# Performance work log

Hardware: AMD Instinct MI355X
Metric: run time of the kernel (lower is better)

## Reference

```python
import jax, jax.numpy as jnp
import numpy as np
from jax.scipy.linalg import expm

N_WIRES = 9
N_LAYERS = 4
EMBED = 512
BATCH = 64
D = 2 ** N_WIRES
P = N_WIRES * N_LAYERS * 2  # gate angles per sample


def _apply_gate(st, g, w):
    # st: (D, 2,...,2) complex64; apply 2x2 gate g on wire w
    st = jnp.moveaxis(st, 1 + w, -1)
    st = st @ g.T  # new[a] = sum_b g[a,b] old[b]
    return jnp.moveaxis(st, -1, 1 + w)


def _apply_cnot(st, c, t):
    st = jnp.moveaxis(st, (1 + c, 1 + t), (-2, -1))
    st = jnp.concatenate([st[..., 0:1, :], st[..., 1:2, ::-1]], axis=-2)
    return jnp.moveaxis(st, (-2, -1), (1 + c, 1 + t))


def _build_unitary(params):
    # simulate circuit on all D basis states at once (identity input)
    st = jnp.eye(D, dtype=jnp.complex64).reshape((D,) + (2,) * N_WIRES)
    idx = 0
    for _ in range(N_LAYERS):
        for w in range(N_WIRES):
            thy = params[idx]
            thz = params[idx + 1]
            idx += 2
            c = jnp.cos(thy * 0.5).astype(jnp.complex64)
            s = jnp.sin(thy * 0.5).astype(jnp.complex64)
            ry = jnp.stack([jnp.stack([c, -s]), jnp.stack([s, c])])
            ep = jnp.exp(0.5j * thz.astype(jnp.complex64))  # exp(i*thz/2)
            zero = jnp.zeros((), jnp.complex64)
            rz = jnp.stack([jnp.stack([jnp.conj(ep), zero]), jnp.stack([zero, ep])])
            st = _apply_gate(st, rz @ ry, w)  # Ry then Rz, fused
        for w in range(N_WIRES - 1):
            st = _apply_cnot(st, w, w + 1)
        st = _apply_cnot(st, N_WIRES - 1, 0)  # ring entangler (n_wires>1)
    # row index = input basis state i -> column i of U; take real part
    return jnp.real(st.reshape(D, D)).T


def _forward(t, w1, b1, w2, b2):
    h = jax.nn.silu(t[:, None] @ w1 + b1)          # (B, EMBED)
    params = h @ w2 + b2                            # (B, P)
    p_sg = jax.lax.stop_gradient(params)            # torch uses .detach() for the circuit
    U_stack = jax.vmap(_build_unitary)(p_sg)        # (B, D, D)
    B = t.shape[0]
    A = jnp.zeros((B, D * D), params.dtype).at[:, :P].set(params).reshape(B, D, D)
    A_skew = (A - jnp.swapaxes(A, -1, -2)) * 0.01
    U_diff = jax.vmap(expm)(A_skew)                 # (B, D, D)
    return jnp.einsum('bij,bjk->bik', U_stack, U_diff)


def setup_inputs() -> dict:
    key = jax.random.key(0)
    k_t, k1, kb1, k2, kb2 = jax.random.split(key, 5)
    t = jax.random.normal(k_t, (BATCH,), jnp.float32)
    w1 = jax.random.normal(k1, (1, EMBED), jnp.float32)
    b1 = jax.random.normal(kb1, (EMBED,), jnp.float32) * 0.1
    w2 = jax.random.normal(k2, (EMBED, P), jnp.float32) / np.sqrt(EMBED)
    b2 = jax.random.normal(kb2, (P,), jnp.float32) * 0.1
    return {"t": t, "w1": w1, "b1": b1, "w2": w2, "b2": b2}


def reference(t, w1, b1, w2, b2):
    return _forward(t, w1, b1, w2, b2)
```

## Files before the change

### kernel.cpp

```cpp
#include <hip/hip_runtime.h>
#include <math.h>


__device__ __forceinline__ float2 cmul(float2 a, float2 b){
  return make_float2(fmaf(a.x, b.x, -a.y*b.y), fmaf(a.x, b.y, a.y*b.x));
}

__device__ __forceinline__ float2 pk_fma_s_lo(float2 s2, float2 b, float2 c){
  float2 d;
  asm("v_pk_fma_f32 %0, %1, %2, %3 op_sel:[0,0,0] op_sel_hi:[0,1,1]"
      : "=v"(d) : "s"(s2), "v"(b), "v"(c));
  return d;
}
__device__ __forceinline__ float2 pk_mul_s_hi(float2 s2, float2 b){
  float2 d;
  asm("v_pk_mul_f32 %0, %1, %2 op_sel:[1,0] op_sel_hi:[1,1]"
      : "=v"(d) : "s"(s2), "v"(b));
  return d;
}
__device__ __forceinline__ float2 pk_fma_vs_lo(float2 a, float2 b, float2 c){
  float2 d;
  asm("v_pk_fma_f32 %0, %1, %2, %3 op_sel:[0,0,0] op_sel_hi:[0,1,1]"
      : "=v"(d) : "v"(a), "s"(b), "v"(c));
  return d;
}
__device__ __forceinline__ float2 pk_mul_vs_hi(float2 a, float2 b){
  float2 d;
  asm("v_pk_mul_f32 %0, %1, %2 op_sel:[1,0] op_sel_hi:[1,1]"
      : "=v"(d) : "v"(a), "s"(b));
  return d;
}
__device__ __forceinline__ float2 pk_fma_vv_lo(float2 a, float2 b, float2 c){
  float2 d;
  asm("v_pk_fma_f32 %0, %1, %2, %3 op_sel:[0,0,0] op_sel_hi:[0,1,1]"
      : "=v"(d) : "v"(a), "v"(b), "v"(c));
  return d;
}
__device__ __forceinline__ float2 pk_mul_vv_hi(float2 a, float2 b){
  float2 d;
  asm("v_pk_mul_f32 %0, %1, %2 op_sel:[1,0] op_sel_hi:[1,1]"
      : "=v"(d) : "v"(a), "v"(b));
  return d;
}
__device__ __forceinline__ float2 pk_swapneg(float2 c, float2 n){
  float2 d;
  asm("v_pk_mul_f32 %0, %1, %2 op_sel:[1,0] op_sel_hi:[0,1]"
      : "=v"(d) : "v"(c), "v"(n));
  return d;
}

__device__ __forceinline__ int Fperm(int x){
  int S = x ^ (x >> 1); S ^= S >> 2; S ^= S >> 4; S ^= S >> 8;
  return (S & 0xFF) | ((((x >> 8) ^ S) & 1) << 8);
}
__device__ __forceinline__ int physmap(int x){ return x ^ ((x >> 4) & 15); }

template<int STRIDE>
__device__ __forceinline__ void apply_rot(float2 amp[8], const float2* rp){
  const float2 R0 = rp[0];
  const float2 R1 = rp[1];
  #pragma unroll
  for (int b = 0; b < 8; ++b){
    if (b & STRIDE) continue;
    const float2 u = amp[b], v = amp[b + STRIDE];
    amp[b]          = pk_fma_s_lo(R0, u, pk_mul_s_hi(R0, v));
    amp[b + STRIDE] = pk_fma_s_lo(R1, u, pk_mul_s_hi(R1, v));
  }
}

__global__ __launch_bounds__(576)
void prep_kernel(const float* __restrict__ t,  const float* __restrict__ w1,
                 const float* __restrict__ b1, const float* __restrict__ w2,
                 const float* __restrict__ b2, float* __restrict__ prep){
  __shared__ float sh[512];
  __shared__ float part[8][72];
  __shared__ float spar[72];
  const int s = blockIdx.x;
  const float ts = t[s];
  for (int k = threadIdx.x; k < 512; k += 576){
    const float z = fmaf(ts, w1[k], b1[k]);
    sh[k] = z / (1.f + expf(-z));
  }
  __syncthreads();
  {
    const int p = threadIdx.x % 72, c = threadIdx.x / 72;
    float acc = 0.f;
    const int k0 = c*64;
    for (int k = k0; k < k0 + 64; ++k) acc = fmaf(sh[k], w2[k*72 + p], acc);
    part[c][p] = acc;
  }
  __syncthreads();
  if (threadIdx.x < 72){
    const int p = threadIdx.x;
    float acc = b2[p];
    #pragma unroll
    for (int c = 0; c < 8; ++c) acc += part[c][p];
    spar[p] = acc;
  }
  __syncthreads();
  float* pb = prep + s*1024;
  const int tid = threadIdx.x;
  if (tid < 192){
    const int l = tid >> 6, m = tid & 63;
    float2 acc = make_float2(1.f, 0.f);
    #pragma unroll
    for (int w = 3; w < 9; ++w){
      const float thz = spar[2*(9*(l+1) + w) + 1];
      float zi, zr; sincosf(0.5f*thz, &zi, &zr);
      const int bit = (m >> (8 - w)) & 1;
      acc = cmul(acc, make_float2(zr, bit ? zi : -zi));
    }
    pb[128 + l*256 + 128 + m*2]     = acc.x;
    pb[128 + l*256 + 128 + m*2 + 1] = acc.y;
  } else if (tid < 216){
    const int q = tid - 192, l = q >> 3, j = q & 7;
    float2 acc = make_float2(1.f, 0.f);
    #pragma unroll
    for (int w = 0; w < 3; ++w){
      const float thz = spar[2*(9*(l+1) + w) + 1];
      float zi, zr; sincosf(0.5f*thz, &zi, &zr);
      const int bit = (j >> (2 - w)) & 1;
      acc = cmul(acc, make_float2(zr, bit ? zi : -zi));
    }
    float* o = pb + 128 + l*256 + 64 + j*4;
    o[0] = acc.x; o[1] = acc.y; o[2] = -acc.y; o[3] = acc.x;
  } else if (tid < 243){
    const int q = tid - 216, l = q / 9, w = q - l*9;
    const float thy = spar[2*(9*(l+1) + w)];
    float sy, cy; sincosf(0.5f*thy, &sy, &cy);
    float* o = pb + 128 + l*256 + w*4;
    o[0] = cy; o[1] = -sy; o[2] = sy; o[3] = cy;
  } else if (tid < 252){
    const int w = tid - 243;
    const float thy = spar[2*w], thz = spar[2*w + 1];
    float sy, cy, zi, zr;
    sincosf(0.5f*thy, &sy, &cy);
    sincosf(0.5f*thz, &zi, &zr);
    float* o = pb + w*8;
    o[0] =  zr*cy; o[1] = -zi*cy;
    o[2] = -zr*sy; o[3] =  zi*sy;
    o[4] =  zr*sy; o[5] =  zi*sy;
    o[6] =  zr*cy; o[7] =  zi*cy;
  } else if (tid < 324){
    const int j = tid - 252;
    pb[896 + j] = (j == 0) ? 0.f : 0.01f*spar[j];
  } else if (tid == 324){
    float th2 = 0.f;
    for (int j = 1; j < 72; ++j){ const float v = 0.01f*spar[j]; th2 = fmaf(v, v, th2); }
    const float th = sqrtf(th2);
    float alpha, beta;
    if (th > 1e-6f){
      alpha = sinf(th)/th;
      const float s2 = sinf(0.5f*th);
      beta = 2.f*s2*s2/th2;
    } else { alpha = 1.f - th2/6.f; beta = 0.5f; }
    pb[968] = cosf(th);
    pb[969] = alpha;
    pb[970] = beta;
  }
}

__global__ __launch_bounds__(512, 8)
void sim_kernel(const float* __restrict__ prep, float* __restrict__ out){
  __shared__ __align__(16) float2 st[8][512];
  const int s    = blockIdx.x & 63;
  const int cb   = blockIdx.x >> 6;
  const int wid  = threadIdx.x >> 6;
  const int lane = threadIdx.x & 63;
  const int col  = cb*8 + wid;
  const float* gp = prep + s*1024;
  float2* const S = st[wid];
  const float2 NEG1P1 = make_float2(-1.f, 1.f);

  float2 amp[8];
  {
    float2 base = make_float2(1.f, 0.f);
    #pragma unroll
    for (int w = 0; w < 6; ++w){
      const int xb = (lane >> (5 - w)) & 1;
      const int ib = (col  >> (8 - w)) & 1;
      const float2 ge = *(const float2*)(gp + 8*w + (xb*2 + ib)*2);
      base = cmul(base, ge);
    }
    const int i6 = (col >> 2) & 1, i7 = (col >> 1) & 1, i8 = col & 1;
    float2 G6[2], G7[2], G8[2];
    #pragma unroll
    for (int r = 0; r < 2; ++r){
      G6[r] = *(const float2*)(gp + 8*6 + (r*2 + i6)*2);
      G7[r] = *(const float2*)(gp + 8*7 + (r*2 + i7)*2);
      G8[r] = *(const float2*)(gp + 8*8 + (r*2 + i8)*2);
    }
    #pragma unroll
    for (int j = 0; j < 8; ++j){
      const float2 tj = cmul(cmul(G6[(j>>2)&1], G7[(j>>1)&1]), G8[j&1]);
      amp[j] = cmul(base, tj);
    }
    const int bFI = physmap(Fperm(lane << 3));
    #pragma unroll
    for (int j = 0; j < 8; ++j) S[bFI ^ physmap(Fperm(j))] = amp[j];
  }

  const int base1 = (lane << 3) ^ ((lane >> 1) & 15);
  const int hq = lane >> 3, lq = lane & 7;
  const int base2 = (hq << 6) ^ ((hq << 2) & 15) ^ lq;
  const int base3 = lane ^ (lane >> 4);
  const int baseF = physmap(Fperm(lane));

  #pragma unroll
  for (int L = 0; L < 3; ++L){
    const float* lb = gp + 128 + L*256;
    #pragma unroll
    for (int j = 0; j < 8; ++j) amp[j] = S[base1 ^ j];
    apply_rot<4>(amp, (const float2*)(lb + 6*4));
    apply_rot<2>(amp, (const float2*)(lb + 7*4));
    apply_rot<1>(amp, (const float2*)(lb + 8*4));
    #pragma unroll
    for (int j = 0; j < 8; ++j) S[base1 ^ j] = amp[j];
    #pragma unroll
    for (int j = 0; j < 8; ++j) amp[j] = S[base2 ^ ((j << 3) ^ (j >> 1))];
    apply_rot<4>(amp, (const float2*)(lb + 3*4));
    apply_rot<2>(amp, (const float2*)(lb + 4*4));
    apply_rot<1>(amp, (const float2*)(lb + 5*4));
    #pragma unroll
    for (int j = 0; j < 8; ++j) S[base2 ^ ((j << 3) ^ (j >> 1))] = amp[j];
    #pragma unroll
    for (int j = 0; j < 8; ++j) amp[j] = S[base3 ^ ((j << 6) ^ ((4*j) & 15))];
    apply_rot<4>(amp, (const float2*)(lb + 0*4));
    apply_rot<2>(amp, (const float2*)(lb + 1*4));
    apply_rot<1>(amp, (const float2*)(lb + 2*4));
    {
      const float2 A = *(const float2*)(lb + 128 + lane*2);
      #pragma unroll
      for (int j = 0; j < 8; ++j){
        const float2 P = *(const float2*)(lb + 64 + j*4);
        const float2 Q = *(const float2*)(lb + 64 + j*4 + 2);
        const float2 C = pk_fma_vs_lo(A, P, pk_mul_vs_hi(A, Q));
        const float2 Dn = pk_swapneg(C, NEG1P1);
        amp[j] = pk_fma_vv_lo(amp[j], C, pk_mul_vv_hi(amp[j], Dn));
      }
    }
    #pragma unroll
    for (int j = 0; j < 8; ++j) S[baseF ^ physmap(Fperm(j << 6))] = amp[j];
  }

  __syncthreads();
  #pragma unroll
  for (int rep = 0; rep < 2; ++rep){
    const int a  = (threadIdx.x >> 1) + rep*256;
    const int q  = threadIdx.x & 1;
    const int pa = a ^ ((a >> 4) & 15);
    float4 vv;
    vv.x = st[q*4 + 0][pa].x;
    vv.y = st[q*4 + 1][pa].x;
    vv.z = st[q*4 + 2][pa].x;
    vv.w = st[q*4 + 3][pa].x;
    *(float4*)&out[(size_t)s*262144 + (size_t)a*512 + cb*8 + q*4] = vv;
  }
}

__global__ __launch_bounds__(288)
void corr_kernel(const float* __restrict__ prep, float* __restrict__ out){
  __shared__ float part[16][18];
  __shared__ float srow[16][2];
  const int s  = blockIdx.x >> 5;
  const int rg = blockIdx.x & 31;
  const float* pp = prep + s*1024;
  const int lr = threadIdx.x / 18;
  const int q  = threadIdx.x - lr*18;
  float* rowp = out + (size_t)s*262144 + (size_t)(rg*16 + lr)*512;
  const float4 x  = *(const float4*)(rowp + q*4);
  const float4 vv = *(const float4*)(pp + 896 + q*4);
  part[lr][q] = fmaf(x.x,vv.x, fmaf(x.y,vv.y, fmaf(x.z,vv.z, x.w*vv.w)));
  __syncthreads();
  if (threadIdx.x < 16){
    const int row = threadIdx.x;
    float uv = 0.f;
    #pragma unroll
    for (int k = 0; k < 18; ++k) uv += part[row][k];
    const float u0 = out[(size_t)s*262144 + (size_t)(rg*16 + row)*512];
    const float cth = pp[968], alpha = pp[969], beta = pp[970];
    srow[row][0] = fmaf(alpha, u0, -beta*uv);
    srow[row][1] = cth*u0 - alpha*uv;
  }
  __syncthreads();
  const float w = srow[lr][0];
  float4 o;
  o.x = fmaf(w, vv.x, x.x); o.y = fmaf(w, vv.y, x.y);
  o.z = fmaf(w, vv.z, x.z); o.w = fmaf(w, vv.w, x.w);
  if (q == 0) o.x = srow[lr][1];
  *(float4*)(rowp + q*4) = o;
}

extern "C" void kernel_launch(void* const* d_in, const int* in_sizes, int n_in,
                              void* d_out, int out_size, void* d_ws, size_t ws_size,
                              hipStream_t stream){
  const float* t  = (const float*)d_in[0];
  const float* w1 = (const float*)d_in[1];
  const float* b1 = (const float*)d_in[2];
  const float* w2 = (const float*)d_in[3];
  const float* b2 = (const float*)d_in[4];
  float* out  = (float*)d_out;
  float* prep = (float*)d_ws;
  prep_kernel<<<64,   576, 0, stream>>>(t, w1, b1, w2, b2, prep);
  sim_kernel <<<4096, 512, 0, stream>>>(prep, out);
  corr_kernel<<<2048, 288, 0, stream>>>(prep, out);
}
```

Before: 148.5 us.

## Fold low-rank expm correction into sim kernel via precomputed U·u and U·v vectors

The prep kernel now simulates the circuit on the two vectors e0 and v, using its own shared-memory state, to get U·e0 and U·v. From these it precomputes per-row correction weights, so the sim kernel can add the rank-2 expm correction directly when it writes the first 72 columns. This removes the separate corr_kernel pass that re-read and rewrote the whole output and needed per-row reductions. It also stores gate entries in a duplicated layout so the sim kernel can use packed FMAs. The cost is more serial work in the 64-block prep kernel and a larger workspace footprint.

```diff
diff --git a/kernel.cpp b/kernel.cpp
--- a/kernel.cpp
+++ b/kernel.cpp
@@ -1,6 +1,14 @@
 #include <hip/hip_runtime.h>
 #include <math.h>
 
+
+#define PSTRIDE 2560
+#define GD_OFF  0
+#define SC_OFF  144
+#define L_OFF(l) (160 + (l)*256)
+#define V_OFF   1184
+#define W_OFF   1280
+#define C0_OFF  1792
 
 __device__ __forceinline__ float2 cmul(float2 a, float2 b){
   return make_float2(fmaf(a.x, b.x, -a.y*b.y), fmaf(a.x, b.y, a.y*b.x));
@@ -55,17 +63,67 @@
 }
 __device__ __forceinline__ int physmap(int x){ return x ^ ((x >> 4) & 15); }
 
-template<int STRIDE>
-__device__ __forceinline__ void apply_rot(float2 amp[8], const float2* rp){
-  const float2 R0 = rp[0];
-  const float2 R1 = rp[1];
+template<int STRIDE, bool UNIF>
+__device__ __forceinline__ void apply_rot(float2 amp[8], const float* rp){
+  const float2 R0 = ((const float2*)rp)[0];
+  const float2 R1 = ((const float2*)rp)[1];
   #pragma unroll
   for (int b = 0; b < 8; ++b){
     if (b & STRIDE) continue;
     const float2 u = amp[b], v = amp[b + STRIDE];
-    amp[b]          = pk_fma_s_lo(R0, u, pk_mul_s_hi(R0, v));
-    amp[b + STRIDE] = pk_fma_s_lo(R1, u, pk_mul_s_hi(R1, v));
-  }
+    if constexpr (UNIF){
+      amp[b]          = pk_fma_s_lo(R0, u, pk_mul_s_hi(R0, v));
+      amp[b + STRIDE] = pk_fma_s_lo(R1, u, pk_mul_s_hi(R1, v));
+    } else {
+      amp[b]          = pk_fma_vv_lo(R0, u, pk_mul_vv_hi(R0, v));
+      amp[b + STRIDE] = pk_fma_vv_lo(R1, u, pk_mul_vv_hi(R1, v));
+    }
+  }
+}
+
+template<bool UNIF>
+__device__ __forceinline__ void run_layer(float2* __restrict__ S,
+    const float* __restrict__ lb, const int lane,
+    const int base1, const int base2, const int base3, const int baseF,
+    const float2 NEG1P1){
+  float2 amp[8];
+  #pragma unroll
+  for (int j = 0; j < 8; ++j) amp[j] = S[base1 ^ j];
+  apply_rot<4, UNIF>(amp, lb + 6*4);
+  apply_rot<2, UNIF>(amp, lb + 7*4);
+  apply_rot<1, UNIF>(amp, lb + 8*4);
+  #pragma unroll
+  for (int j = 0; j < 8; ++j) S[base1 ^ j] = amp[j];
+  #pragma unroll
+  for (int j = 0; j < 8; ++j) amp[j] = S[base2 ^ ((j << 3) ^ (j >> 1))];
+  apply_rot<4, UNIF>(amp, lb + 3*4);
+  apply_rot<2, UNIF>(amp, lb + 4*4);
+  apply_rot<1, UNIF>(amp, lb + 5*4);
+  #pragma unroll
+  for (int j = 0; j < 8; ++j) S[base2 ^ ((j << 3) ^ (j >> 1))] = amp[j];
+  #pragma unroll
+  for (int j = 0; j < 8; ++j) amp[j] = S[base3 ^ ((j << 6) ^ ((4*j) & 15))];
+  apply_rot<4, UNIF>(amp, lb + 0*4);
+  apply_rot<2, UNIF>(amp, lb + 1*4);
+  apply_rot<1, UNIF>(amp, lb + 2*4);
+  {
+    const float2 A  = *(const float2*)(lb + 128 + lane*2);
+    const float2 A2 = pk_swapneg(A, NEG1P1);
+    #pragma unroll
+    for (int j = 0; j < 8; ++j)
+      amp[j] = pk_fma_vv_lo(amp[j], A, pk_mul_vv_hi(amp[j], A2));
+    #pragma unroll
+    for (int j = 0; j < 8; ++j){
+      const float2 P = *(const float2*)(lb + 64 + j*4);
+      const float2 Q = *(const float2*)(lb + 64 + j*4 + 2);
+      if constexpr (UNIF)
+        amp[j] = pk_fma_vs_lo(amp[j], P, pk_mul_vs_hi(amp[j], Q));
+      else
+        amp[j] = pk_fma_vv_lo(amp[j], P, pk_mul_vv_hi(amp[j], Q));
+    }
+  }
+  #pragma unroll
+  for (int j = 0; j < 8; ++j) S[baseF ^ physmap(Fperm(j << 6))] = amp[j];
 }
 
 __global__ __launch_bounds__(576)
@@ -75,6 +133,9 @@
   __shared__ float sh[512];
   __shared__ float part[8][72];
   __shared__ float spar[72];
+  __shared__ float tl[4][256];
+  __shared__ float ssc[3];
+  __shared__ __align__(16) float2 vst[2][512];
   const int s = blockIdx.x;
   const float ts = t[s];
   for (int k = threadIdx.x; k < 512; k += 576){
@@ -98,53 +159,61 @@
     spar[p] = acc;
   }
   __syncthreads();
-  float* pb = prep + s*1024;
+  float* pb = prep + (size_t)s*PSTRIDE;
   const int tid = threadIdx.x;
-  if (tid < 192){
+  if (tid < 256){
     const int l = tid >> 6, m = tid & 63;
     float2 acc = make_float2(1.f, 0.f);
     #pragma unroll
     for (int w = 3; w < 9; ++w){
-      const float thz = spar[2*(9*(l+1) + w) + 1];
+      const float thz = spar[2*(9*l + w) + 1];
       float zi, zr; sincosf(0.5f*thz, &zi, &zr);
       const int bit = (m >> (8 - w)) & 1;
       acc = cmul(acc, make_float2(zr, bit ? zi : -zi));
     }
-    pb[128 + l*256 + 128 + m*2]     = acc.x;
-    pb[128 + l*256 + 128 + m*2 + 1] = acc.y;
-  } else if (tid < 216){
-    const int q = tid - 192, l = q >> 3, j = q & 7;
+    pb[L_OFF(l) + 128 + 2*m]     = acc.x;
+    pb[L_OFF(l) + 128 + 2*m + 1] = acc.y;
+    tl[l][128 + 2*m]     = acc.x;
+    tl[l][128 + 2*m + 1] = acc.y;
+  } else if (tid < 288){
+    const int q = tid - 256, l = q >> 3, j = q & 7;
     float2 acc = make_float2(1.f, 0.f);
     #pragma unroll
     for (int w = 0; w < 3; ++w){
-      const float thz = spar[2*(9*(l+1) + w) + 1];
+      const float thz = spar[2*(9*l + w) + 1];
       float zi, zr; sincosf(0.5f*thz, &zi, &zr);
       const int bit = (j >> (2 - w)) & 1;
       acc = cmul(acc, make_float2(zr, bit ? zi : -zi));
     }
-    float* o = pb + 128 + l*256 + 64 + j*4;
+    float* o = pb + L_OFF(l) + 64 + j*4;
     o[0] = acc.x; o[1] = acc.y; o[2] = -acc.y; o[3] = acc.x;
-  } else if (tid < 243){
-    const int q = tid - 216, l = q / 9, w = q - l*9;
-    const float thy = spar[2*(9*(l+1) + w)];
+    float* o2 = &tl[l][64 + j*4];
+    o2[0] = acc.x; o2[1] = acc.y; o2[2] = -acc.y; o2[3] = acc.x;
+  } else if (tid < 324){
+    const int q = tid - 288, l = q / 9, w = q - l*9;
+    const float thy = spar[2*(9*l + w)];
     float sy, cy; sincosf(0.5f*thy, &sy, &cy);
-    float* o = pb + 128 + l*256 + w*4;
+    float* o = pb + L_OFF(l) + w*4;
     o[0] = cy; o[1] = -sy; o[2] = sy; o[3] = cy;
-  } else if (tid < 252){
-    const int w = tid - 243;
+    float* o2 = &tl[l][w*4];
+    o2[0] = cy; o2[1] = -sy; o2[2] = sy; o2[3] = cy;
+  } else if (tid < 333){
+    const int w = tid - 324;
     const float thy = spar[2*w], thz = spar[2*w + 1];
     float sy, cy, zi, zr;
     sincosf(0.5f*thy, &sy, &cy);
     sincosf(0.5f*thz, &zi, &zr);
-    float* o = pb + w*8;
-    o[0] =  zr*cy; o[1] = -zi*cy;
-    o[2] = -zr*sy; o[3] =  zi*sy;
-    o[4] =  zr*sy; o[5] =  zi*sy;
-    o[6] =  zr*cy; o[7] =  zi*cy;
-  } else if (tid < 324){
-    const int j = tid - 252;
-    pb[896 + j] = (j == 0) ? 0.f : 0.01f*spar[j];
-  } else if (tid == 324){
+    const float gr[4] = { zr*cy, -zr*sy, zr*sy, zr*cy };
+    const float gi[4] = { -zi*cy, zi*sy, zi*sy, zi*cy };
+    float* o = pb + GD_OFF + w*16;
+    #pragma unroll
+    for (int e = 0; e < 4; ++e){
+      o[e*4+0] = gr[e]; o[e*4+1] = gi[e]; o[e*4+2] = -gi[e]; o[e*4+3] = gr[e];
+    }
+  } else if (tid < 405){
+    const int j = tid - 333;
+    pb[V_OFF + j] = (j == 0) ? 0.f : 0.01f*spar[j];
+  } else if (tid == 405){
     float th2 = 0.f;
     for (int j = 1; j < 72; ++j){ const float v = 0.01f*spar[j]; th2 = fmaf(v, v, th2); }
     const float th = sqrtf(th2);
@@ -154,9 +223,41 @@
       const float s2 = sinf(0.5f*th);
       beta = 2.f*s2*s2/th2;
     } else { alpha = 1.f - th2/6.f; beta = 0.5f; }
-    pb[968] = cosf(th);
-    pb[969] = alpha;
-    pb[970] = beta;
+    pb[SC_OFF+0] = cosf(th);
+    pb[SC_OFF+1] = alpha;
+    pb[SC_OFF+2] = beta;
+    ssc[0] = cosf(th); ssc[1] = alpha; ssc[2] = beta;
+  }
+  __syncthreads();
+  if (tid < 128){
+    const int wv = tid >> 6, lane = tid & 63;
+    float2* const S = vst[wv];
+    const float2 NEG1P1 = make_float2(-1.f, 1.f);
+    const int base1 = (lane << 3) ^ ((lane >> 1) & 15);
+    const int hq = lane >> 3, lq = lane & 7;
+    const int base2 = (hq << 6) ^ ((hq << 2) & 15) ^ lq;
+    const int base3 = lane ^ (lane >> 4);
+    const int baseF = physmap(Fperm(lane));
+    #pragma unroll
+    for (int j = 0; j < 8; ++j){
+      const int x = (lane << 3) + j;
+      float re;
+      if (wv == 0) re = (x == 0) ? 1.f : 0.f;
+      else         re = (x >= 1 && x < 72) ? 0.01f*spar[x] : 0.f;
+      S[base1 ^ j] = make_float2(re, 0.f);
+    }
+    #pragma unroll
+    for (int L = 0; L < 4; ++L)
+      run_layer<false>(S, &tl[L][0], lane, base1, base2, base3, baseF, NEG1P1);
+  }
+  __syncthreads();
+  if (tid < 512){
+    const int a  = tid;
+    const int pa = a ^ ((a >> 4) & 15);
+    const float u0 = vst[0][pa].x;
+    const float uv = vst[1][pa].x;
+    pb[W_OFF  + a] = fmaf(ssc[1], u0, -ssc[2]*uv);
+    pb[C0_OFF + a] = fmaf(ssc[0], u0, -ssc[1]*uv);
   }
 }
 
@@ -168,7 +269,7 @@
   const int wid  = threadIdx.x >> 6;
   const int lane = threadIdx.x & 63;
   const int col  = cb*8 + wid;
-  const float* gp = prep + s*1024;
+  const float* gp = prep + (size_t)s*PSTRIDE;
   float2* const S = st[wid];
   const float2 NEG1P1 = make_float2(-1.f, 1.f);
 
@@ -179,21 +280,37 @@
     for (int w = 0; w < 6; ++w){
       const int xb = (lane >> (5 - w)) & 1;
       const int ib = (col  >> (8 - w)) & 1;
-      const float2 ge = *(const float2*)(gp + 8*w + (xb*2 + ib)*2);
-      base = cmul(base, ge);
+      const float4 gd = *(const float4*)(gp + GD_OFF + w*16 + (xb*2 + ib)*4);
+      const float2 d1 = make_float2(gd.x, gd.y);
+      const float2 d2 = make_float2(gd.z, gd.w);
+      base = pk_fma_vv_lo(base, d1, pk_mul_vv_hi(base, d2));
     }
     const int i6 = (col >> 2) & 1, i7 = (col >> 1) & 1, i8 = col & 1;
-    float2 G6[2], G7[2], G8[2];
+    float2 g6[2]; float4 g7d[2], g8d[2];
     #pragma unroll
     for (int r = 0; r < 2; ++r){
-      G6[r] = *(const float2*)(gp + 8*6 + (r*2 + i6)*2);
-      G7[r] = *(const float2*)(gp + 8*7 + (r*2 + i7)*2);
-      G8[r] = *(const float2*)(gp + 8*8 + (r*2 + i8)*2);
-    }
+      g6[r]  = *(const float2*)(gp + GD_OFF + 6*16 + (r*2 + i6)*4);
+      g7d[r] = *(const float4*)(gp + GD_OFF + 7*16 + (r*2 + i7)*4);
+      g8d[r] = *(const float4*)(gp + GD_OFF + 8*16 + (r*2 + i8)*4);
+    }
+    float2 g67[4];
+    #pragma unroll
+    for (int a = 0; a < 2; ++a){
+      #pragma unroll
+      for (int b = 0; b < 2; ++b){
+        const float2 d1 = make_float2(g7d[b].x, g7d[b].y);
+        const float2 d2 = make_float2(g7d[b].z, g7d[b].w);
+        g67[a*2+b] = pk_fma_vv_lo(g6[a], d1, pk_mul_vv_hi(g6[a], d2));
+      }
+    }
+    const float2 bd2 = pk_swapneg(base, NEG1P1);
     #pragma unroll
     for (int j = 0; j < 8; ++j){
-      const float2 tj = cmul(cmul(G6[(j>>2)&1], G7[(j>>1)&1]), G8[j&1]);
-      amp[j] = cmul(base, tj);
+      const float4 g8 = g8d[j & 1];
+      const float2 e1 = make_float2(g8.x, g8.y);
+      const float2 e2 = make_float2(g8.z, g8.w);
+      const float2 T  = pk_fma_vv_lo(g67[j >> 1], e1, pk_mul_vv_hi(g67[j >> 1], e2));
+      amp[j] = pk_fma_vv_lo(T, base, pk_mul_vv_hi(T, bd2));
     }
     const int bFI = physmap(Fperm(lane << 3));
     #pragma unroll
@@ -206,44 +323,14 @@
   const int base3 = lane ^ (lane >> 4);
   const int baseF = physmap(Fperm(lane));
 
-  #pragma unroll
-  for (int L = 0; L < 3; ++L){
-    const float* lb = gp + 128 + L*256;
-    #pragma unroll
-    for (int j = 0; j < 8; ++j) amp[j] = S[base1 ^ j];
-    apply_rot<4>(amp, (const float2*)(lb + 6*4));
-    apply_rot<2>(amp, (const float2*)(lb + 7*4));
-    apply_rot<1>(amp, (const float2*)(lb + 8*4));
-    #pragma unroll
-    for (int j = 0; j < 8; ++j) S[base1 ^ j] = amp[j];
-    #pragma unroll
-    for (int j = 0; j < 8; ++j) amp[j] = S[base2 ^ ((j << 3) ^ (j >> 1))];
-    apply_rot<4>(amp, (const float2*)(lb + 3*4));
-    apply_rot<2>(amp, (const float2*)(lb + 4*4));
-    apply_rot<1>(amp, (const float2*)(lb + 5*4));
-    #pragma unroll
-    for (int j = 0; j < 8; ++j) S[base2 ^ ((j << 3) ^ (j >> 1))] = amp[j];
-    #pragma unroll
-    for (int j = 0; j < 8; ++j) amp[j] = S[base3 ^ ((j << 6) ^ ((4*j) & 15))];
-    apply_rot<4>(amp, (const float2*)(lb + 0*4));
-    apply_rot<2>(amp, (const float2*)(lb + 1*4));
-    apply_rot<1>(amp, (const float2*)(lb + 2*4));
-    {
-      const float2 A = *(const float2*)(lb + 128 + lane*2);
-      #pragma unroll
-      for (int j = 0; j < 8; ++j){
-        const float2 P = *(const float2*)(lb + 64 + j*4);
-        const float2 Q = *(const float2*)(lb + 64 + j*4 + 2);
-        const float2 C = pk_fma_vs_lo(A, P, pk_mul_vs_hi(A, Q));
-        const float2 Dn = pk_swapneg(C, NEG1P1);
-        amp[j] = pk_fma_vv_lo(amp[j], C, pk_mul_vv_hi(amp[j], Dn));
-      }
-    }
-    #pragma unroll
-    for (int j = 0; j < 8; ++j) S[baseF ^ physmap(Fperm(j << 6))] = amp[j];
-  }
-
-  __syncthreads();
+  run_layer<true>(S, gp + L_OFF(1), lane, base1, base2, base3, baseF, NEG1P1);
+  run_layer<true>(S, gp + L_OFF(2), lane, base1, base2, base3, baseF, NEG1P1);
+  run_layer<true>(S, gp + L_OFF(3), lane, base1, base2, base3, baseF, NEG1P1);
+
+  __syncthreads();
+  const float* wt  = gp + W_OFF;
+  const float* c0t = gp + C0_OFF;
+  const float* vt  = gp + V_OFF;
   #pragma unroll
   for (int rep = 0; rep < 2; ++rep){
     const int a  = (threadIdx.x >> 1) + rep*256;
@@ -254,41 +341,17 @@
     vv.y = st[q*4 + 1][pa].x;
     vv.z = st[q*4 + 2][pa].x;
     vv.w = st[q*4 + 3][pa].x;
+    if (cb < 9){
+      const float  wa = wt[a];
+      const float4 vj = *(const float4*)(vt + cb*8 + q*4);
+      vv.x = fmaf(wa, vj.x, vv.x);
+      vv.y = fmaf(wa, vj.y, vv.y);
+      vv.z = fmaf(wa, vj.z, vv.z);
+      vv.w = fmaf(wa, vj.w, vv.w);
+      if ((cb | q) == 0) vv.x = c0t[a];
+    }
     *(float4*)&out[(size_t)s*262144 + (size_t)a*512 + cb*8 + q*4] = vv;
   }
-}
-
-__global__ __launch_bounds__(288)
-void corr_kernel(const float* __restrict__ prep, float* __restrict__ out){
-  __shared__ float part[16][18];
-  __shared__ float srow[16][2];
-  const int s  = blockIdx.x >> 5;
-  const int rg = blockIdx.x & 31;
-  const float* pp = prep + s*1024;
-  const int lr = threadIdx.x / 18;
-  const int q  = threadIdx.x - lr*18;
-  float* rowp = out + (size_t)s*262144 + (size_t)(rg*16 + lr)*512;
-  const float4 x  = *(const float4*)(rowp + q*4);
-  const float4 vv = *(const float4*)(pp + 896 + q*4);
-  part[lr][q] = fmaf(x.x,vv.x, fmaf(x.y,vv.y, fmaf(x.z,vv.z, x.w*vv.w)));
-  __syncthreads();
-  if (threadIdx.x < 16){
-    const int row = threadIdx.x;
-    float uv = 0.f;
-    #pragma unroll
-    for (int k = 0; k < 18; ++k) uv += part[row][k];
-    const float u0 = out[(size_t)s*262144 + (size_t)(rg*16 + row)*512];
-    const float cth = pp[968], alpha = pp[969], beta = pp[970];
-    srow[row][0] = fmaf(alpha, u0, -beta*uv);
-    srow[row][1] = cth*u0 - alpha*uv;
-  }
-  __syncthreads();
-  const float w = srow[lr][0];
-  float4 o;
-  o.x = fmaf(w, vv.x, x.x); o.y = fmaf(w, vv.y, x.y);
-  o.z = fmaf(w, vv.z, x.z); o.w = fmaf(w, vv.w, x.w);
-  if (q == 0) o.x = srow[lr][1];
-  *(float4*)(rowp + q*4) = o;
 }
 
 extern "C" void kernel_launch(void* const* d_in, const int* in_sizes, int n_in,
@@ -303,5 +366,4 @@
   float* prep = (float*)d_ws;
   prep_kernel<<<64,   576, 0, stream>>>(t, w1, b1, w2, b2, prep);
   sim_kernel <<<4096, 512, 0, stream>>>(prep, out);
-  corr_kernel<<<2048, 288, 0, stream>>>(prep, out);
-}
+}
```

After: 144.9 us. 2.4% less time.
